# Performance work log

Hardware: AMD Instinct MI355X
Metric: run time of the kernel (lower is better)

## Reference

```python
import jax, jax.numpy as jnp
import numpy as np

B, T, DM = 2, 512, 1024
H, DH = 16, 64          # n_heads, d_head = d_model // n_heads
D, R = 32, 4            # d_manifold, metric_net rank
TEMP_MIN = 0.5


def _rope_tables(t_len, d_head):
    inv_freq = 1.0 / (10000.0 ** (jnp.arange(0, d_head, 2, dtype=jnp.float32) / d_head))
    t = jnp.arange(t_len, dtype=jnp.float32)
    freqs = t[:, None] * inv_freq[None, :]          # [T, d_head//2]
    emb = jnp.concatenate([freqs, freqs], axis=-1)  # [T, d_head]
    return jnp.cos(emb), jnp.sin(emb)


def _apply_rope(x, cos, sin):
    # x: [B, H, T, d_head]
    half = x.shape[-1] // 2
    x1, x2 = x[..., :half], x[..., half:]
    c1 = cos[None, None, :, :half]
    s1 = sin[None, None, :, :half]
    return jnp.concatenate([x1 * c1 - x2 * s1, x1 * s1 + x2 * c1], axis=-1)


def setup_inputs() -> dict:
    key = jax.random.key(0)
    ks = jax.random.split(key, 9)
    s = 0.02
    return {
        "x": jax.random.normal(ks[0], (B, T, DM), dtype=jnp.float32),
        "Wq": s * jax.random.normal(ks[1], (DM, DM), dtype=jnp.float32),
        "Wk": s * jax.random.normal(ks[2], (DM, DM), dtype=jnp.float32),
        "Wv": s * jax.random.normal(ks[3], (DM, DM), dtype=jnp.float32),
        "Wo": s * jax.random.normal(ks[4], (DM, DM), dtype=jnp.float32),
        "Wqm": s * jax.random.normal(ks[5], (DH, D), dtype=jnp.float32),
        "Wkm": s * jax.random.normal(ks[6], (DH, D), dtype=jnp.float32),
        "Wmetric": s * jax.random.normal(ks[7], (D, D * R), dtype=jnp.float32),
        "temperature": jnp.asarray(1.0, dtype=jnp.float32),
    }


def reference(x, Wq, Wk, Wv, Wo, Wqm, Wkm, Wmetric, temperature):
    b, t, c = x.shape
    # projections -> [B, H, T, d_head]
    def split_heads(y):
        return y.reshape(b, t, H, DH).transpose(0, 2, 1, 3)
    q = split_heads(x @ Wq)
    k = split_heads(x @ Wk)
    v = split_heads(x @ Wv)

    cos, sin = _rope_tables(t, DH)
    q = _apply_rope(q, cos, sin)
    k = _apply_rope(k, cos, sin)

    # manifold coordinates in (0,1): [B, H, T, D]
    qm = jax.nn.sigmoid(jnp.einsum('bhtd,dm->bhtm', q, Wqm))
    km = jax.nn.sigmoid(jnp.einsum('bhtd,dm->bhtm', k, Wkm))

    # low-rank metric factor U(q): [B, H, T, D, R]
    U = jnp.einsum('bhtm,mn->bhtn', qm, Wmetric).reshape(b, H, t, D, R)

    # Euclidean part: ||q_i - k_j||^2 = |q|^2 + |k|^2 - 2 q.k  -> [B,H,T,T]
    q2 = jnp.sum(qm * qm, axis=-1)
    k2 = jnp.sum(km * km, axis=-1)
    qk = jnp.einsum('bhid,bhjd->bhij', qm, km)
    dist_euc = q2[..., :, None] + k2[..., None, :] - 2.0 * qk

    # low-rank part: ||U_i^T (q_i - k_j)||^2, factorized as U_i^T q_i - U_i^T k_j
    Uq = jnp.einsum('bhidr,bhid->bhir', U, qm)          # [B,H,T,R]
    Uk = jnp.einsum('bhidr,bhjd->bhijr', U, km)         # [B,H,T,T,R]
    dist_lr = jnp.sum((Uq[:, :, :, None, :] - Uk) ** 2, axis=-1)

    dist_sq = jnp.maximum(dist_euc + dist_lr, 0.0)

    temp = jnp.maximum(temperature, TEMP_MIN)
    attn = -dist_sq / temp

    causal = jnp.triu(jnp.ones((t, t), dtype=bool), k=1)
    attn = jnp.where(causal[None, None], -jnp.inf, attn)
    attn = jax.nn.softmax(attn, axis=-1)

    out = jnp.einsum('bhij,bhjd->bhid', attn, v)        # [B,H,T,d_head]
    out = out.transpose(0, 2, 1, 3).reshape(b, t, c)
    return out @ Wo
```

## Files before the change

kernel.cpp:

```cpp
#include <hip/hip_runtime.h>
#include <cmath>

constexpr int B_  = 2;
constexpr int T_  = 512;
constexpr int DM_ = 1024;
constexpr int H_  = 16;
constexpr int DH_ = 64;
constexpr int D_  = 32;
constexpr int R_  = 4;
constexpr int BH_ = B_ * H_;

typedef __bf16 bf16x8 __attribute__((ext_vector_type(8)));
typedef float  f32x4  __attribute__((ext_vector_type(4)));
typedef unsigned short u16x8 __attribute__((ext_vector_type(8)));

__device__ __forceinline__ unsigned short f2bf(float f) {
    unsigned u = __float_as_uint(f);
    return (unsigned short)((u + 0x7fffu + ((u >> 16) & 1u)) >> 16);
}
__device__ __forceinline__ float bf2f(unsigned short v) {
    return __uint_as_float((unsigned)v << 16);
}
__device__ __forceinline__ void gload16(const void* g, void* l) {
    __builtin_amdgcn_global_load_lds(
        (const __attribute__((address_space(1))) void*)g,
        (__attribute__((address_space(3))) void*)l, 16, 0, 0);
}

__global__ __launch_bounds__(256) void prep_kernel(
    const float* __restrict__ x,
    const float* __restrict__ Wq, const float* __restrict__ Wk,
    const float* __restrict__ Wv, const float* __restrict__ Wo,
    unsigned short* __restrict__ xb,
    unsigned short* __restrict__ wqb, unsigned short* __restrict__ wkb,
    unsigned short* __restrict__ wvb, unsigned short* __restrict__ wob)
{
    const int t = threadIdx.x;
    const int z = blockIdx.z;
    if (z == 4) {
        int base = (blockIdx.y * 16 + blockIdx.x) * 4096 + t * 16;
#pragma unroll
        for (int c = 0; c < 4; ++c) {
            float4 v = *(const float4*)&x[base + c * 4];
            ushort4 o = { f2bf(v.x), f2bf(v.y), f2bf(v.z), f2bf(v.w) };
            *(ushort4*)&xb[base + c * 4] = o;
        }
        return;
    }
    __shared__ __align__(16) unsigned short Ls[64][72];
    const float* W = (z == 0) ? Wq : (z == 1) ? Wk : (z == 2) ? Wv : Wo;
    unsigned short* O = (z == 0) ? wqb : (z == 1) ? wkb : (z == 2) ? wvb : wob;
    const int k0 = blockIdx.x * 64;
    const int n0 = blockIdx.y * 64;
#pragma unroll
    for (int it = 0; it < 4; ++it) {
        int r = it * 16 + (t >> 4);
        int c = (t & 15) * 4;
        float4 v4 = *(const float4*)&W[(size_t)(k0 + r) * DM_ + n0 + c];
        Ls[c + 0][r] = f2bf(v4.x); Ls[c + 1][r] = f2bf(v4.y);
        Ls[c + 2][r] = f2bf(v4.z); Ls[c + 3][r] = f2bf(v4.w);
    }
    __syncthreads();
#pragma unroll
    for (int it = 0; it < 2; ++it) {
        int nl = it * 32 + (t >> 3);
        int kc = (t & 7) * 8;
        *(u16x8*)&O[(size_t)(n0 + nl) * DM_ + k0 + kc] = *(const u16x8*)&Ls[nl][kc];
    }
}

template <int EPI>
__global__ __launch_bounds__(256) void mfma_gemm_db(
    const unsigned short* __restrict__ A,
    const unsigned short* __restrict__ Bt0,
    const unsigned short* __restrict__ Bt1,
    const unsigned short* __restrict__ Bt2,
    float* __restrict__ C0, float* __restrict__ C1,
    unsigned short* __restrict__ vT)
{
    __shared__ __align__(16) unsigned short As[2][64 * 64];
    __shared__ __align__(16) unsigned short Bs[2][64 * 64];
    const int tid  = threadIdx.x;
    const int lane = tid & 63;
    const int w    = tid >> 6;
    const int wm   = (w & 1) * 32;
    const int wn   = (w >> 1) * 32;
    const int l15  = lane & 15, quad = lane >> 4;

    const int bm = blockIdx.y * 64;
    int bn, which = 0;
    const unsigned short* Bt;
    if (EPI == 0) {
        int n0 = blockIdx.x * 64;
        which = n0 >> 10;
        bn = n0 & 1023;
        Bt = (which == 0) ? Bt0 : (which == 1) ? Bt1 : Bt2;
    } else {
        bn = blockIdx.x * 64;
        Bt = Bt0;
    }

    const int srow = tid >> 3, kcs = tid & 7, kcg = kcs ^ (srow & 7);
    const unsigned short* Ap0 = A  + (size_t)(bm + srow) * DM_ + kcg * 8;
    const unsigned short* Bp0 = Bt + (size_t)(bn + srow) * DM_ + kcg * 8;
    const unsigned short* Ap1 = Ap0 + 32 * DM_;
    const unsigned short* Bp1 = Bp0 + 32 * DM_;

    gload16(Ap0, &As[0][tid * 8]);
    gload16(Ap1, &As[0][tid * 8 + 2048]);
    gload16(Bp0, &Bs[0][tid * 8]);
    gload16(Bp1, &Bs[0][tid * 8 + 2048]);

    f32x4 acc[2][2] = {};
#pragma unroll
    for (int k = 0; k < 16; ++k) {
        const int cur = k & 1, nxt = cur ^ 1;
        __builtin_amdgcn_s_barrier();
        if (k + 1 < 16) {
            const int off = (k + 1) * 64;
            gload16(Ap0 + off, &As[nxt][tid * 8]);
            gload16(Ap1 + off, &As[nxt][tid * 8 + 2048]);
            gload16(Bp0 + off, &Bs[nxt][tid * 8]);
            gload16(Bp1 + off, &Bs[nxt][tid * 8 + 2048]);
            __builtin_amdgcn_s_waitcnt(0x0F74);
        } else {
            __builtin_amdgcn_s_waitcnt(0x0F70);
        }
        __builtin_amdgcn_s_barrier();

        bf16x8 af[2][2], bfr[2][2];
#pragma unroll
        for (int ki = 0; ki < 2; ++ki)
#pragma unroll
            for (int i = 0; i < 2; ++i) {
                int ra = wm + i * 16 + l15;
                int rb = wn + i * 16 + l15;
                int kch = ki * 4 + quad;
                af[ki][i]  = *(const bf16x8*)&As[cur][ra * 64 + (kch ^ (ra & 7)) * 8];
                bfr[ki][i] = *(const bf16x8*)&Bs[cur][rb * 64 + (kch ^ (rb & 7)) * 8];
            }
#pragma unroll
        for (int mi = 0; mi < 2; ++mi)
#pragma unroll
            for (int ni = 0; ni < 2; ++ni) {
                acc[mi][ni] = __builtin_amdgcn_mfma_f32_16x16x32_bf16(
                    af[0][mi], bfr[0][ni], acc[mi][ni], 0, 0, 0);
                acc[mi][ni] = __builtin_amdgcn_mfma_f32_16x16x32_bf16(
                    af[1][mi], bfr[1][ni], acc[mi][ni], 0, 0, 0);
            }
    }

#pragma unroll
    for (int mi = 0; mi < 2; ++mi)
#pragma unroll
        for (int ni = 0; ni < 2; ++ni) {
            f32x4 a = acc[mi][ni];
            int col = wn + ni * 16 + l15;
#pragma unroll
            for (int r = 0; r < 4; ++r) {
                int row = bm + wm + mi * 16 + quad * 4 + r;
                if (EPI == 0) {
                    int h = bn >> 6, d = col;
                    int bb = row >> 9, tt = row & (T_ - 1);
                    if (which == 2) {
                        vT[(((size_t)bb * H_ + h) * DH_ + d) * T_ + tt] = f2bf(a[r]);
                    } else {
                        float* C = (which == 0) ? C0 : C1;
                        C[(((size_t)bb * H_ + h) * T_ + tt) * DH_ + d] = a[r];
                    }
                } else {
                    C0[(size_t)row * DM_ + bn + col] = a[r];
                }
            }
        }
}

__global__ __launch_bounds__(256) void feat_both(
    const float* __restrict__ q_raw, const float* __restrict__ k_raw,
    const float* __restrict__ Wqm,   const float* __restrict__ Wkm,
    const float* __restrict__ Wmetric,
    unsigned short* __restrict__ a_hi, unsigned short* __restrict__ a_lo,
    unsigned short* __restrict__ km_hi, unsigned short* __restrict__ km_lo,
    float* __restrict__ q2p, float* __restrict__ k2,
    unsigned short* __restrict__ Urb)
{
    const bool QSIDE = (blockIdx.y == 0);
    const float* raw = QSIDE ? q_raw : k_raw;
    const float* Wm  = QSIDE ? Wqm   : Wkm;

    __shared__ float qrs[4][64];
    __shared__ float qms[4][32];
    __shared__ float Us[4][128];
    __shared__ float Uqs[4][4];
    const int tid  = threadIdx.x;
    const int w    = tid >> 6;
    const int lane = tid & 63;
    const int row  = blockIdx.x * 4 + w;
    const int t    = row & (T_ - 1);
    const int bh   = row >> 9;

    float rv = raw[(size_t)row * 64 + lane];
    int   fi = lane & 31;
    float ang = (float)t * expf((float)fi * -0.28782313662425575f);
    float s, c;
    sincosf(ang, &s, &c);
    float partner = __shfl_xor(rv, 32);
    float qr = (lane < 32) ? (rv * c - partner * s) : (partner * s + rv * c);
    qrs[w][lane] = qr;
    __syncthreads();

    if (lane < 32) {
        float acc = 0.f;
#pragma unroll 8
        for (int d = 0; d < 64; ++d) acc += qrs[w][d] * Wm[d * 32 + lane];
        qms[w][lane] = 1.0f / (1.0f + __expf(-acc));
    }
    __syncthreads();

    if (QSIDE) {
        float a0 = 0.f, a1 = 0.f;
#pragma unroll 8
        for (int m = 0; m < 32; ++m) {
            float qv = qms[w][m];
            a0 += qv * Wmetric[m * 128 + lane];
            a1 += qv * Wmetric[m * 128 + 64 + lane];
        }
        Us[w][lane] = a0; Us[w][64 + lane] = a1;
        {
            int r0 = lane & 3, d0 = lane >> 2;
            int d1 = 16 + (lane >> 2);
            Urb[(((size_t)bh * R_ + r0) * T_ + t) * D_ + d0] = f2bf(a0);
            Urb[(((size_t)bh * R_ + r0) * T_ + t) * D_ + d1] = f2bf(a1);
        }
        __syncthreads();
        if (lane < 4) {
            float acc = 0.f;
#pragma unroll
            for (int d = 0; d < 32; ++d) acc += Us[w][d * 4 + lane] * qms[w][d];
            Uqs[w][lane] = acc;
        }
        __syncthreads();
        if (lane < 32) {
            float b = Uqs[w][0] * Us[w][lane * 4 + 0]
                    + Uqs[w][1] * Us[w][lane * 4 + 1]
                    + Uqs[w][2] * Us[w][lane * 4 + 2]
                    + Uqs[w][3] * Us[w][lane * 4 + 3];
            float a = qms[w][lane] + b;
            unsigned short hi = f2bf(a);
            unsigned short lo = f2bf(a - bf2f(hi));
            size_t off = (size_t)row * 32 + lane;
            a_hi[off] = hi; a_lo[off] = lo;
        }
        if (lane == 0) {
            float acc = 0.f;
#pragma unroll
            for (int m = 0; m < 32; ++m) acc += qms[w][m] * qms[w][m];
#pragma unroll
            for (int r = 0; r < 4; ++r) acc += Uqs[w][r] * Uqs[w][r];
            q2p[row] = acc;
        }
    } else {
        if (lane < 32) {
            float v = qms[w][lane];
            unsigned short hi = f2bf(v);
            unsigned short lo = f2bf(v - bf2f(hi));
            size_t off = (size_t)row * 32 + lane;
            km_hi[off] = hi; km_lo[off] = lo;
        }
        if (lane == 0) {
            float acc = 0.f;
#pragma unroll
            for (int m = 0; m < 32; ++m) acc += qms[w][m] * qms[w][m];
            k2[row] = acc;
        }
    }
}

constexpr int PROW = 40;
__global__ __launch_bounds__(256) void attn_mfma(
    const unsigned short* __restrict__ a_hi, const unsigned short* __restrict__ a_lo,
    const unsigned short* __restrict__ km_hi, const unsigned short* __restrict__ km_lo,
    const unsigned short* __restrict__ Urb,
    const float* __restrict__ q2p, const float* __restrict__ k2,
    const float* __restrict__ temp_p, const unsigned short* __restrict__ vT,
    unsigned short* __restrict__ ctxb)
{
    __shared__ __align__(16) unsigned short P_lds[4][32 * PROW];
    __shared__ __align__(16) float OP[4][32][64];
    __shared__ float ML[4][32];

    const int itile = blockIdx.x, bh = blockIdx.y;
    const int i0 = itile * 32;
    const int tid = threadIdx.x, w = tid >> 6, lane = tid & 63;
    const int l15 = lane & 15, quad = lane >> 4;

    const float inv_temp = 1.0f / fmaxf(temp_p[0], 0.5f);

    bf16x8 Ahi[2], Alo[2], Aur[4][2];
#pragma unroll
    for (int mi = 0; mi < 2; ++mi) {
        size_t ab = ((size_t)bh * T_ + i0 + mi * 16 + l15) * 32 + quad * 8;
        Ahi[mi] = *(const bf16x8*)&a_hi[ab];
        Alo[mi] = *(const bf16x8*)&a_lo[ab];
#pragma unroll
        for (int r = 0; r < 4; ++r)
            Aur[r][mi] = *(const bf16x8*)
                &Urb[(((size_t)bh * R_ + r) * T_ + i0 + mi * 16 + l15) * 32 + quad * 8];
    }
    float q2r[2][4];
#pragma unroll
    for (int mi = 0; mi < 2; ++mi)
#pragma unroll
        for (int rg = 0; rg < 4; ++rg)
            q2r[mi][rg] = q2p[(size_t)bh * T_ + i0 + mi * 16 + quad * 4 + rg];

    f32x4 Oacc[2][4] = {};
    float psum[2][4] = {};

    for (int jt = w; jt <= itile; jt += 4) {
        const int j0 = jt * 32;
        bf16x8 Bhi[2], Blo[2];
#pragma unroll
        for (int ni = 0; ni < 2; ++ni) {
            size_t kb = ((size_t)bh * T_ + j0 + ni * 16 + l15) * 32 + quad * 8;
            Bhi[ni] = *(const bf16x8*)&km_hi[kb];
            Blo[ni] = *(const bf16x8*)&km_lo[kb];
        }
        f32x4 acc[2][2] = {};
#pragma unroll
        for (int mi = 0; mi < 2; ++mi)
#pragma unroll
            for (int ni = 0; ni < 2; ++ni) {
                acc[mi][ni] = __builtin_amdgcn_mfma_f32_16x16x32_bf16(
                    Alo[mi], Bhi[ni], acc[mi][ni], 0, 0, 0);
                acc[mi][ni] = __builtin_amdgcn_mfma_f32_16x16x32_bf16(
                    Ahi[mi], Blo[ni], acc[mi][ni], 0, 0, 0);
                acc[mi][ni] = __builtin_amdgcn_mfma_f32_16x16x32_bf16(
                    Ahi[mi], Bhi[ni], acc[mi][ni], 0, 0, 0);
            }
        f32x4 sq[2][2] = {};
#pragma unroll
        for (int r = 0; r < 4; ++r) {
            f32x4 ar[2][2] = {};
#pragma unroll
            for (int mi = 0; mi < 2; ++mi)
#pragma unroll
                for (int ni = 0; ni < 2; ++ni)
                    ar[mi][ni] = __builtin_amdgcn_mfma_f32_16x16x32_bf16(
                        Aur[r][mi], Bhi[ni], ar[mi][ni], 0, 0, 0);
#pragma unroll
            for (int mi = 0; mi < 2; ++mi)
#pragma unroll
                for (int ni = 0; ni < 2; ++ni)
                    sq[mi][ni] += ar[mi][ni] * ar[mi][ni];
        }
        float k2c[2];
#pragma unroll
        for (int ni = 0; ni < 2; ++ni)
            k2c[ni] = k2[(size_t)bh * T_ + j0 + ni * 16 + l15];
        const bool diag = (jt == itile);
#pragma unroll
        for (int mi = 0; mi < 2; ++mi)
#pragma unroll
            for (int ni = 0; ni < 2; ++ni)
#pragma unroll
                for (int rg = 0; rg < 4; ++rg) {
                    float dist = q2r[mi][rg] + k2c[ni]
                               - 2.f * acc[mi][ni][rg] + sq[mi][ni][rg];
                    float sc = -fmaxf(dist, 0.f) * inv_temp;
                    if (diag && (ni * 16 + l15) > (mi * 16 + quad * 4 + rg))
                        sc = -1e30f;
                    float p = __expf(sc);
                    psum[mi][rg] += p;
                    P_lds[w][(mi * 16 + quad * 4 + rg) * PROW + ni * 16 + l15] = f2bf(p);
                }
        bf16x8 Pf[2], Vf[4];
#pragma unroll
        for (int mi = 0; mi < 2; ++mi)
            Pf[mi] = *(const bf16x8*)&P_lds[w][(mi * 16 + l15) * PROW + quad * 8];
#pragma unroll
        for (int n4 = 0; n4 < 4; ++n4)
            Vf[n4] = *(const bf16x8*)
                &vT[((size_t)bh * DH_ + n4 * 16 + l15) * T_ + j0 + quad * 8];
#pragma unroll
        for (int mi = 0; mi < 2; ++mi)
#pragma unroll
            for (int n4 = 0; n4 < 4; ++n4)
                Oacc[mi][n4] = __builtin_amdgcn_mfma_f32_16x16x32_bf16(
                    Pf[mi], Vf[n4], Oacc[mi][n4], 0, 0, 0);
    }

#pragma unroll
    for (int mi = 0; mi < 2; ++mi)
#pragma unroll
        for (int rg = 0; rg < 4; ++rg) {
            float v = psum[mi][rg];
            v += __shfl_xor(v, 1); v += __shfl_xor(v, 2);
            v += __shfl_xor(v, 4); v += __shfl_xor(v, 8);
            psum[mi][rg] = v;
        }
    if (l15 == 0)
#pragma unroll
        for (int mi = 0; mi < 2; ++mi)
#pragma unroll
            for (int rg = 0; rg < 4; ++rg)
                ML[w][mi * 16 + quad * 4 + rg] = psum[mi][rg];
#pragma unroll
    for (int mi = 0; mi < 2; ++mi)
#pragma unroll
        for (int n4 = 0; n4 < 4; ++n4)
#pragma unroll
            for (int rg = 0; rg < 4; ++rg)
                OP[w][mi * 16 + quad * 4 + rg][n4 * 16 + l15] = Oacc[mi][n4][rg];
    __syncthreads();

    const int ii = tid >> 3, ds = tid & 7;
    float l = ML[0][ii] + ML[1][ii] + ML[2][ii] + ML[3][ii];
    float O[8] = {};
#pragma unroll
    for (int wv = 0; wv < 4; ++wv) {
        float4 o0 = *(const float4*)&OP[wv][ii][ds * 8];
        float4 o1 = *(const float4*)&OP[wv][ii][ds * 8 + 4];
        O[0] += o0.x; O[1] += o0.y; O[2] += o0.z; O[3] += o0.w;
        O[4] += o1.x; O[5] += o1.y; O[6] += o1.z; O[7] += o1.w;
    }
    const float inv = 1.0f / l;
    const int b = bh >> 4, h = bh & 15;
    u16x8 o;
#pragma unroll
    for (int dd = 0; dd < 8; ++dd) o[dd] = f2bf(O[dd] * inv);
    *(u16x8*)&ctxb[((size_t)b * T_ + i0 + ii) * DM_ + h * 64 + ds * 8] = o;
}

extern "C" void kernel_launch(void* const* d_in, const int* in_sizes, int n_in,
                              void* d_out, int out_size, void* d_ws, size_t ws_size,
                              hipStream_t stream)
{
    const float* x       = (const float*)d_in[0];
    const float* Wq      = (const float*)d_in[1];
    const float* Wk      = (const float*)d_in[2];
    const float* Wv      = (const float*)d_in[3];
    const float* Wo      = (const float*)d_in[4];
    const float* Wqm     = (const float*)d_in[5];
    const float* Wkm     = (const float*)d_in[6];
    const float* Wmetric = (const float*)d_in[7];
    const float* temp    = (const float*)d_in[8];
    float* out = (float*)d_out;
    float* ws  = (float*)d_ws;

    float* q_raw = ws;
    float* k_raw = q_raw + (size_t)BH_ * T_ * DH_;
    float* q2p   = k_raw + (size_t)BH_ * T_ * DH_;
    float* k2    = q2p   + (size_t)BH_ * T_;
    unsigned short* xb   = (unsigned short*)(k2 + (size_t)BH_ * T_);
    unsigned short* wqb  = xb   + (size_t)DM_ * DM_;
    unsigned short* wkb  = wqb  + (size_t)DM_ * DM_;
    unsigned short* wvb  = wkb  + (size_t)DM_ * DM_;
    unsigned short* wob  = wvb  + (size_t)DM_ * DM_;
    unsigned short* a_hi = wob  + (size_t)DM_ * DM_;
    unsigned short* a_lo = a_hi + (size_t)BH_ * T_ * D_;
    unsigned short* kmhi = a_lo + (size_t)BH_ * T_ * D_;
    unsigned short* kmlo = kmhi + (size_t)BH_ * T_ * D_;
    unsigned short* Urb  = kmlo + (size_t)BH_ * T_ * D_;
    unsigned short* vT   = Urb  + (size_t)BH_ * R_ * T_ * D_;
    unsigned short* ctxb = (unsigned short*)q_raw;

    prep_kernel<<<dim3(16, 16, 5), 256, 0, stream>>>(
        x, Wq, Wk, Wv, Wo, xb, wqb, wkb, wvb, wob);
    mfma_gemm_db<0><<<dim3(48, 16), 256, 0, stream>>>(
        xb, wqb, wkb, wvb, q_raw, k_raw, vT);
    feat_both<<<dim3(BH_ * T_ / 4, 2), 256, 0, stream>>>(
        q_raw, k_raw, Wqm, Wkm, Wmetric,
        a_hi, a_lo, kmhi, kmlo, q2p, k2, Urb);
    attn_mfma<<<dim3(T_ / 32, BH_), 256, 0, stream>>>(
        a_hi, a_lo, kmhi, kmlo, Urb, q2p, k2, temp, vT, ctxb);
    mfma_gemm_db<1><<<dim3(16, 16), 256, 0, stream>>>(
        ctxb, wob, nullptr, nullptr, out, nullptr, nullptr);
}
```

Measured before the change: 146.9 us.

## Split-K the Q/K projection GEMM and sum partials in feature kernel

The Q and K projection GEMM tiles are split into two K-halves, each writing a separate fp32 partial buffer. The V tiles keep the full K loop. This raises the grid from 768 to 1280 blocks to fill more compute units. The feature kernel adds the two partials when it loads raw q/k. The cost is extra workspace, double the fp32 writes for q/k, and an extra read in the feature kernel. The K loop is no longer fully unrolled because the iteration count is now a runtime value.

```diff
diff --git a/kernel.cpp b/kernel.cpp
--- a/kernel.cpp
+++ b/kernel.cpp
@@ -69,13 +69,12 @@
     }
 }
 
-template <int EPI>
-__global__ __launch_bounds__(256) void mfma_gemm_db(
+__global__ __launch_bounds__(256) void qkv_gemm_ksplit(
     const unsigned short* __restrict__ A,
-    const unsigned short* __restrict__ Bt0,
-    const unsigned short* __restrict__ Bt1,
-    const unsigned short* __restrict__ Bt2,
-    float* __restrict__ C0, float* __restrict__ C1,
+    const unsigned short* __restrict__ wqb, const unsigned short* __restrict__ wkb,
+    const unsigned short* __restrict__ wvb,
+    float* __restrict__ q_rawA, float* __restrict__ q_rawB,
+    float* __restrict__ k_rawA, float* __restrict__ k_rawB,
     unsigned short* __restrict__ vT)
 {
     __shared__ __align__(16) unsigned short As[2][64 * 64];
@@ -88,17 +87,365 @@
     const int l15  = lane & 15, quad = lane >> 4;
 
     const int bm = blockIdx.y * 64;
-    int bn, which = 0;
-    const unsigned short* Bt;
-    if (EPI == 0) {
-        int n0 = blockIdx.x * 64;
+    const int u  = blockIdx.x;
+    int which, bn, k_begin, k_iters;
+    float* Cout = nullptr;
+    if (u < 64) {
+        int qk = u >> 1, half = u & 1;
+        int n0 = qk * 64;
         which = n0 >> 10;
         bn = n0 & 1023;
-        Bt = (which == 0) ? Bt0 : (which == 1) ? Bt1 : Bt2;
+        k_begin = half * 512;
+        k_iters = 8;
+        Cout = (which == 0) ? (half ? q_rawB : q_rawA)
+                            : (half ? k_rawB : k_rawA);
     } else {
-        bn = blockIdx.x * 64;
-        Bt = Bt0;
-    }
+        which = 2; bn = (u - 64) * 64; k_begin = 0; k_iters = 16;
+    }
+    const unsigned short* Bt = (which == 0) ? wqb : (which == 1) ? wkb : wvb;
+
+    const int srow = tid >> 3, kcs = tid & 7, kcg = kcs ^ (srow & 7);
+    const unsigned short* Ap0 = A  + (size_t)(bm + srow) * DM_ + kcg * 8 + k_begin;
+    const unsigned short* Bp0 = Bt + (size_t)(bn + srow) * DM_ + kcg * 8 + k_begin;
+    const unsigned short* Ap1 = Ap0 + 32 * DM_;
+    const unsigned short* Bp1 = Bp0 + 32 * DM_;
+
+    gload16(Ap0, &As[0][tid * 8]);
+    gload16(Ap1, &As[0][tid * 8 + 2048]);
+    gload16(Bp0, &Bs[0][tid * 8]);
+    gload16(Bp1, &Bs[0][tid * 8 + 2048]);
+
+    f32x4 acc[2][2] = {};
+    for (int k = 0; k < k_iters; ++k) {
+        const int cur = k & 1, nxt = cur ^ 1;
+        __builtin_amdgcn_s_barrier();
+        if (k + 1 < k_iters) {
+            const int off = (k + 1) * 64;
+            gload16(Ap0 + off, &As[nxt][tid * 8]);
+            gload16(Ap1 + off, &As[nxt][tid * 8 + 2048]);
+            gload16(Bp0 + off, &Bs[nxt][tid * 8]);
+            gload16(Bp1 + off, &Bs[nxt][tid * 8 + 2048]);
+            __builtin_amdgcn_s_waitcnt(0x0F74);
+        } else {
+            __builtin_amdgcn_s_waitcnt(0x0F70);
+        }
+        __builtin_amdgcn_s_barrier();
+
+        bf16x8 af[2][2], bfr[2][2];
+#pragma unroll
+        for (int ki = 0; ki < 2; ++ki)
+#pragma unroll
+            for (int i = 0; i < 2; ++i) {
+                int ra = wm + i * 16 + l15;
+                int rb = wn + i * 16 + l15;
+                int kch = ki * 4 + quad;
+                af[ki][i]  = *(const bf16x8*)&As[cur][ra * 64 + (kch ^ (ra & 7)) * 8];
+                bfr[ki][i] = *(const bf16x8*)&Bs[cur][rb * 64 + (kch ^ (rb & 7)) * 8];
+            }
+#pragma unroll
+        for (int mi = 0; mi < 2; ++mi)
+#pragma unroll
+            for (int ni = 0; ni < 2; ++ni) {
+                acc[mi][ni] = __builtin_amdgcn_mfma_f32_16x16x32_bf16(
+                    af[0][mi], bfr[0][ni], acc[mi][ni], 0, 0, 0);
+                acc[mi][ni] = __builtin_amdgcn_mfma_f32_16x16x32_bf16(
+                    af[1][mi], bfr[1][ni], acc[mi][ni], 0, 0, 0);
+            }
+    }
+
+    const int h = bn >> 6;
+#pragma unroll
+    for (int mi = 0; mi < 2; ++mi)
+#pragma unroll
+        for (int ni = 0; ni < 2; ++ni) {
+            f32x4 a = acc[mi][ni];
+            int d = wn + ni * 16 + l15;
+#pragma unroll
+            for (int r = 0; r < 4; ++r) {
+                int row = bm + wm + mi * 16 + quad * 4 + r;
+                int bb = row >> 9, tt = row & (T_ - 1);
+                if (which == 2) {
+                    vT[(((size_t)bb * H_ + h) * DH_ + d) * T_ + tt] = f2bf(a[r]);
+                } else {
+                    Cout[(((size_t)bb * H_ + h) * T_ + tt) * DH_ + d] = a[r];
+                }
+            }
+        }
+}
+
+__global__ __launch_bounds__(256) void feat_both(
+    const float* __restrict__ q_rawA, const float* __restrict__ q_rawB,
+    const float* __restrict__ k_rawA, const float* __restrict__ k_rawB,
+    const float* __restrict__ Wqm,   const float* __restrict__ Wkm,
+    const float* __restrict__ Wmetric,
+    unsigned short* __restrict__ a_hi, unsigned short* __restrict__ a_lo,
+    unsigned short* __restrict__ km_hi, unsigned short* __restrict__ km_lo,
+    float* __restrict__ q2p, float* __restrict__ k2,
+    unsigned short* __restrict__ Urb)
+{
+    const bool QSIDE = (blockIdx.y == 0);
+    const float* rawA = QSIDE ? q_rawA : k_rawA;
+    const float* rawB = QSIDE ? q_rawB : k_rawB;
+    const float* Wm   = QSIDE ? Wqm   : Wkm;
+
+    __shared__ float qrs[4][64];
+    __shared__ float qms[4][32];
+    __shared__ float Us[4][128];
+    __shared__ float Uqs[4][4];
+    const int tid  = threadIdx.x;
+    const int w    = tid >> 6;
+    const int lane = tid & 63;
+    const int row  = blockIdx.x * 4 + w;
+    const int t    = row & (T_ - 1);
+    const int bh   = row >> 9;
+
+    float rv = rawA[(size_t)row * 64 + lane] + rawB[(size_t)row * 64 + lane];
+    int   fi = lane & 31;
+    float ang = (float)t * expf((float)fi * -0.28782313662425575f);
+    float s, c;
+    sincosf(ang, &s, &c);
+    float partner = __shfl_xor(rv, 32);
+    float qr = (lane < 32) ? (rv * c - partner * s) : (partner * s + rv * c);
+    qrs[w][lane] = qr;
+    __syncthreads();
+
+    if (lane < 32) {
+        float acc = 0.f;
+#pragma unroll 8
+        for (int d = 0; d < 64; ++d) acc += qrs[w][d] * Wm[d * 32 + lane];
+        qms[w][lane] = 1.0f / (1.0f + __expf(-acc));
+    }
+    __syncthreads();
+
+    if (QSIDE) {
+        float a0 = 0.f, a1 = 0.f;
+#pragma unroll 8
+        for (int m = 0; m < 32; ++m) {
+            float qv = qms[w][m];
+            a0 += qv * Wmetric[m * 128 + lane];
+            a1 += qv * Wmetric[m * 128 + 64 + lane];
+        }
+        Us[w][lane] = a0; Us[w][64 + lane] = a1;
+        {
+            int r0 = lane & 3, d0 = lane >> 2;
+            int d1 = 16 + (lane >> 2);
+            Urb[(((size_t)bh * R_ + r0) * T_ + t) * D_ + d0] = f2bf(a0);
+            Urb[(((size_t)bh * R_ + r0) * T_ + t) * D_ + d1] = f2bf(a1);
+        }
+        __syncthreads();
+        if (lane < 4) {
+            float acc = 0.f;
+#pragma unroll
+            for (int d = 0; d < 32; ++d) acc += Us[w][d * 4 + lane] * qms[w][d];
+            Uqs[w][lane] = acc;
+        }
+        __syncthreads();
+        if (lane < 32) {
+            float b = Uqs[w][0] * Us[w][lane * 4 + 0]
+                    + Uqs[w][1] * Us[w][lane * 4 + 1]
+                    + Uqs[w][2] * Us[w][lane * 4 + 2]
+                    + Uqs[w][3] * Us[w][lane * 4 + 3];
+            float a = qms[w][lane] + b;
+            unsigned short hi = f2bf(a);
+            unsigned short lo = f2bf(a - bf2f(hi));
+            size_t off = (size_t)row * 32 + lane;
+            a_hi[off] = hi; a_lo[off] = lo;
+        }
+        if (lane == 0) {
+            float acc = 0.f;
+#pragma unroll
+            for (int m = 0; m < 32; ++m) acc += qms[w][m] * qms[w][m];
+#pragma unroll
+            for (int r = 0; r < 4; ++r) acc += Uqs[w][r] * Uqs[w][r];
+            q2p[row] = acc;
+        }
+    } else {
+        if (lane < 32) {
+            float v = qms[w][lane];
+            unsigned short hi = f2bf(v);
+            unsigned short lo = f2bf(v - bf2f(hi));
+            size_t off = (size_t)row * 32 + lane;
+            km_hi[off] = hi; km_lo[off] = lo;
+        }
+        if (lane == 0) {
+            float acc = 0.f;
+#pragma unroll
+            for (int m = 0; m < 32; ++m) acc += qms[w][m] * qms[w][m];
+            k2[row] = acc;
+        }
+    }
+}
+
+constexpr int PROW = 40;
+__global__ __launch_bounds__(256) void attn_mfma(
+    const unsigned short* __restrict__ a_hi, const unsigned short* __restrict__ a_lo,
+    const unsigned short* __restrict__ km_hi, const unsigned short* __restrict__ km_lo,
+    const unsigned short* __restrict__ Urb,
+    const float* __restrict__ q2p, const float* __restrict__ k2,
+    const float* __restrict__ temp_p, const unsigned short* __restrict__ vT,
+    unsigned short* __restrict__ ctxb)
+{
+    __shared__ __align__(16) unsigned short P_lds[4][32 * PROW];
+    __shared__ __align__(16) float OP[4][32][64];
+    __shared__ float ML[4][32];
+
+    const int itile = blockIdx.x, bh = blockIdx.y;
+    const int i0 = itile * 32;
+    const int tid = threadIdx.x, w = tid >> 6, lane = tid & 63;
+    const int l15 = lane & 15, quad = lane >> 4;
+
+    const float inv_temp = 1.0f / fmaxf(temp_p[0], 0.5f);
+
+    bf16x8 Ahi[2], Alo[2], Aur[4][2];
+#pragma unroll
+    for (int mi = 0; mi < 2; ++mi) {
+        size_t ab = ((size_t)bh * T_ + i0 + mi * 16 + l15) * 32 + quad * 8;
+        Ahi[mi] = *(const bf16x8*)&a_hi[ab];
+        Alo[mi] = *(const bf16x8*)&a_lo[ab];
+#pragma unroll
+        for (int r = 0; r < 4; ++r)
+            Aur[r][mi] = *(const bf16x8*)
+                &Urb[(((size_t)bh * R_ + r) * T_ + i0 + mi * 16 + l15) * 32 + quad * 8];
+    }
+    float q2r[2][4];
+#pragma unroll
+    for (int mi = 0; mi < 2; ++mi)
+#pragma unroll
+        for (int rg = 0; rg < 4; ++rg)
+            q2r[mi][rg] = q2p[(size_t)bh * T_ + i0 + mi * 16 + quad * 4 + rg];
+
+    f32x4 Oacc[2][4] = {};
+    float psum[2][4] = {};
+
+    for (int jt = w; jt <= itile; jt += 4) {
+        const int j0 = jt * 32;
+        bf16x8 Bhi[2], Blo[2];
+#pragma unroll
+        for (int ni = 0; ni < 2; ++ni) {
+            size_t kb = ((size_t)bh * T_ + j0 + ni * 16 + l15) * 32 + quad * 8;
+            Bhi[ni] = *(const bf16x8*)&km_hi[kb];
+            Blo[ni] = *(const bf16x8*)&km_lo[kb];
+        }
+        f32x4 acc[2][2] = {};
+#pragma unroll
+        for (int mi = 0; mi < 2; ++mi)
+#pragma unroll
+            for (int ni = 0; ni < 2; ++ni) {
+                acc[mi][ni] = __builtin_amdgcn_mfma_f32_16x16x32_bf16(
+                    Alo[mi], Bhi[ni], acc[mi][ni], 0, 0, 0);
+                acc[mi][ni] = __builtin_amdgcn_mfma_f32_16x16x32_bf16(
+                    Ahi[mi], Blo[ni], acc[mi][ni], 0, 0, 0);
+                acc[mi][ni] = __builtin_amdgcn_mfma_f32_16x16x32_bf16(
+                    Ahi[mi], Bhi[ni], acc[mi][ni], 0, 0, 0);
+            }
+        f32x4 sq[2][2] = {};
+#pragma unroll
+        for (int r = 0; r < 4; ++r) {
+            f32x4 ar[2][2] = {};
+#pragma unroll
+            for (int mi = 0; mi < 2; ++mi)
+#pragma unroll
+                for (int ni = 0; ni < 2; ++ni)
+                    ar[mi][ni] = __builtin_amdgcn_mfma_f32_16x16x32_bf16(
+                        Aur[r][mi], Bhi[ni], ar[mi][ni], 0, 0, 0);
+#pragma unroll
+            for (int mi = 0; mi < 2; ++mi)
+#pragma unroll
+                for (int ni = 0; ni < 2; ++ni)
+                    sq[mi][ni] += ar[mi][ni] * ar[mi][ni];
+        }
+        float k2c[2];
+#pragma unroll
+        for (int ni = 0; ni < 2; ++ni)
+            k2c[ni] = k2[(size_t)bh * T_ + j0 + ni * 16 + l15];
+        const bool diag = (jt == itile);
+#pragma unroll
+        for (int mi = 0; mi < 2; ++mi)
+#pragma unroll
+            for (int ni = 0; ni < 2; ++ni)
+#pragma unroll
+                for (int rg = 0; rg < 4; ++rg) {
+                    float dist = q2r[mi][rg] + k2c[ni]
+                               - 2.f * acc[mi][ni][rg] + sq[mi][ni][rg];
+                    float sc = -fmaxf(dist, 0.f) * inv_temp;
+                    if (diag && (ni * 16 + l15) > (mi * 16 + quad * 4 + rg))
+                        sc = -1e30f;
+                    float p = __expf(sc);
+                    psum[mi][rg] += p;
+                    P_lds[w][(mi * 16 + quad * 4 + rg) * PROW + ni * 16 + l15] = f2bf(p);
+                }
+        bf16x8 Pf[2], Vf[4];
+#pragma unroll
+        for (int mi = 0; mi < 2; ++mi)
+            Pf[mi] = *(const bf16x8*)&P_lds[w][(mi * 16 + l15) * PROW + quad * 8];
+#pragma unroll
+        for (int n4 = 0; n4 < 4; ++n4)
+            Vf[n4] = *(const bf16x8*)
+                &vT[((size_t)bh * DH_ + n4 * 16 + l15) * T_ + j0 + quad * 8];
+#pragma unroll
+        for (int mi = 0; mi < 2; ++mi)
+#pragma unroll
+            for (int n4 = 0; n4 < 4; ++n4)
+                Oacc[mi][n4] = __builtin_amdgcn_mfma_f32_16x16x32_bf16(
+                    Pf[mi], Vf[n4], Oacc[mi][n4], 0, 0, 0);
+    }
+
+#pragma unroll
+    for (int mi = 0; mi < 2; ++mi)
+#pragma unroll
+        for (int rg = 0; rg < 4; ++rg) {
+            float v = psum[mi][rg];
+            v += __shfl_xor(v, 1); v += __shfl_xor(v, 2);
+            v += __shfl_xor(v, 4); v += __shfl_xor(v, 8);
+            psum[mi][rg] = v;
+        }
+    if (l15 == 0)
+#pragma unroll
+        for (int mi = 0; mi < 2; ++mi)
+#pragma unroll
+            for (int rg = 0; rg < 4; ++rg)
+                ML[w][mi * 16 + quad * 4 + rg] = psum[mi][rg];
+#pragma unroll
+    for (int mi = 0; mi < 2; ++mi)
+#pragma unroll
+        for (int n4 = 0; n4 < 4; ++n4)
+#pragma unroll
+            for (int rg = 0; rg < 4; ++rg)
+                OP[w][mi * 16 + quad * 4 + rg][n4 * 16 + l15] = Oacc[mi][n4][rg];
+    __syncthreads();
+
+    const int ii = tid >> 3, ds = tid & 7;
+    float l = ML[0][ii] + ML[1][ii] + ML[2][ii] + ML[3][ii];
+    float O[8] = {};
+#pragma unroll
+    for (int wv = 0; wv < 4; ++wv) {
+        float4 o0 = *(const float4*)&OP[wv][ii][ds * 8];
+        float4 o1 = *(const float4*)&OP[wv][ii][ds * 8 + 4];
+        O[0] += o0.x; O[1] += o0.y; O[2] += o0.z; O[3] += o0.w;
+        O[4] += o1.x; O[5] += o1.y; O[6] += o1.z; O[7] += o1.w;
+    }
+    const float inv = 1.0f / l;
+    const int b = bh >> 4, h = bh & 15;
+    u16x8 o;
+#pragma unroll
+    for (int dd = 0; dd < 8; ++dd) o[dd] = f2bf(O[dd] * inv);
+    *(u16x8*)&ctxb[((size_t)b * T_ + i0 + ii) * DM_ + h * 64 + ds * 8] = o;
+}
+
+__global__ __launch_bounds__(256) void out_gemm_db(
+    const unsigned short* __restrict__ A, const unsigned short* __restrict__ Bt,
+    float* __restrict__ C)
+{
+    __shared__ __align__(16) unsigned short As[2][64 * 64];
+    __shared__ __align__(16) unsigned short Bs[2][64 * 64];
+    const int tid  = threadIdx.x;
+    const int lane = tid & 63;
+    const int w    = tid >> 6;
+    const int wm   = (w & 1) * 32;
+    const int wn   = (w >> 1) * 32;
+    const int l15  = lane & 15, quad = lane >> 4;
+    const int bm = blockIdx.y * 64;
+    const int bn = blockIdx.x * 64;
 
     const int srow = tid >> 3, kcs = tid & 7, kcg = kcs ^ (srow & 7);
     const unsigned short* Ap0 = A  + (size_t)(bm + srow) * DM_ + kcg * 8;
@@ -112,7 +459,6 @@
     gload16(Bp1, &Bs[0][tid * 8 + 2048]);
 
     f32x4 acc[2][2] = {};
-#pragma unroll
     for (int k = 0; k < 16; ++k) {
         const int cur = k & 1, nxt = cur ^ 1;
         __builtin_amdgcn_s_barrier();
@@ -149,287 +495,18 @@
                     af[1][mi], bfr[1][ni], acc[mi][ni], 0, 0, 0);
             }
     }
-
 #pragma unroll
     for (int mi = 0; mi < 2; ++mi)
 #pragma unroll
         for (int ni = 0; ni < 2; ++ni) {
             f32x4 a = acc[mi][ni];
-            int col = wn + ni * 16 + l15;
+            int col = bn + wn + ni * 16 + l15;
 #pragma unroll
             for (int r = 0; r < 4; ++r) {
                 int row = bm + wm + mi * 16 + quad * 4 + r;
-                if (EPI == 0) {
-                    int h = bn >> 6, d = col;
-                    int bb = row >> 9, tt = row & (T_ - 1);
-                    if (which == 2) {
-                        vT[(((size_t)bb * H_ + h) * DH_ + d) * T_ + tt] = f2bf(a[r]);
-                    } else {
-                        float* C = (which == 0) ? C0 : C1;
-                        C[(((size_t)bb * H_ + h) * T_ + tt) * DH_ + d] = a[r];
-                    }
-                } else {
-                    C0[(size_t)row * DM_ + bn + col] = a[r];
-                }
-            }
-        }
-}
-
-__global__ __launch_bounds__(256) void feat_both(
-    const float* __restrict__ q_raw, const float* __restrict__ k_raw,
-    const float* __restrict__ Wqm,   const float* __restrict__ Wkm,
-    const float* __restrict__ Wmetric,
-    unsigned short* __restrict__ a_hi, unsigned short* __restrict__ a_lo,
-    unsigned short* __restrict__ km_hi, unsigned short* __restrict__ km_lo,
-    float* __restrict__ q2p, float* __restrict__ k2,
-    unsigned short* __restrict__ Urb)
-{
-    const bool QSIDE = (blockIdx.y == 0);
-    const float* raw = QSIDE ? q_raw : k_raw;
-    const float* Wm  = QSIDE ? Wqm   : Wkm;
-
-    __shared__ float qrs[4][64];
-    __shared__ float qms[4][32];
-    __shared__ float Us[4][128];
-    __shared__ float Uqs[4][4];
-    const int tid  = threadIdx.x;
-    const int w    = tid >> 6;
-    const int lane = tid & 63;
-    const int row  = blockIdx.x * 4 + w;
-    const int t    = row & (T_ - 1);
-    const int bh   = row >> 9;
-
-    float rv = raw[(size_t)row * 64 + lane];
-    int   fi = lane & 31;
-    float ang = (float)t * expf((float)fi * -0.28782313662425575f);
-    float s, c;
-    sincosf(ang, &s, &c);
-    float partner = __shfl_xor(rv, 32);
-    float qr = (lane < 32) ? (rv * c - partner * s) : (partner * s + rv * c);
-    qrs[w][lane] = qr;
-    __syncthreads();
-
-    if (lane < 32) {
-        float acc = 0.f;
-#pragma unroll 8
-        for (int d = 0; d < 64; ++d) acc += qrs[w][d] * Wm[d * 32 + lane];
-        qms[w][lane] = 1.0f / (1.0f + __expf(-acc));
-    }
-    __syncthreads();
-
-    if (QSIDE) {
-        float a0 = 0.f, a1 = 0.f;
-#pragma unroll 8
-        for (int m = 0; m < 32; ++m) {
-            float qv = qms[w][m];
-            a0 += qv * Wmetric[m * 128 + lane];
-            a1 += qv * Wmetric[m * 128 + 64 + lane];
-        }
-        Us[w][lane] = a0; Us[w][64 + lane] = a1;
-        {
-            int r0 = lane & 3, d0 = lane >> 2;
-            int d1 = 16 + (lane >> 2);
-            Urb[(((size_t)bh * R_ + r0) * T_ + t) * D_ + d0] = f2bf(a0);
-            Urb[(((size_t)bh * R_ + r0) * T_ + t) * D_ + d1] = f2bf(a1);
-        }
-        __syncthreads();
-        if (lane < 4) {
-            float acc = 0.f;
-#pragma unroll
-            for (int d = 0; d < 32; ++d) acc += Us[w][d * 4 + lane] * qms[w][d];
-            Uqs[w][lane] = acc;
-        }
-        __syncthreads();
-        if (lane < 32) {
-            float b = Uqs[w][0] * Us[w][lane * 4 + 0]
-                    + Uqs[w][1] * Us[w][lane * 4 + 1]
-                    + Uqs[w][2] * Us[w][lane * 4 + 2]
-                    + Uqs[w][3] * Us[w][lane * 4 + 3];
-            float a = qms[w][lane] + b;
-            unsigned short hi = f2bf(a);
-            unsigned short lo = f2bf(a - bf2f(hi));
-            size_t off = (size_t)row * 32 + lane;
-            a_hi[off] = hi; a_lo[off] = lo;
-        }
-        if (lane == 0) {
-            float acc = 0.f;
-#pragma unroll
-            for (int m = 0; m < 32; ++m) acc += qms[w][m] * qms[w][m];
-#pragma unroll
-            for (int r = 0; r < 4; ++r) acc += Uqs[w][r] * Uqs[w][r];
-            q2p[row] = acc;
-        }
-    } else {
-        if (lane < 32) {
-            float v = qms[w][lane];
-            unsigned short hi = f2bf(v);
-            unsigned short lo = f2bf(v - bf2f(hi));
-            size_t off = (size_t)row * 32 + lane;
-            km_hi[off] = hi; km_lo[off] = lo;
-        }
-        if (lane == 0) {
-            float acc = 0.f;
-#pragma unroll
-            for (int m = 0; m < 32; ++m) acc += qms[w][m] * qms[w][m];
-            k2[row] = acc;
-        }
-    }
-}
-
-constexpr int PROW = 40;
-__global__ __launch_bounds__(256) void attn_mfma(
-    const unsigned short* __restrict__ a_hi, const unsigned short* __restrict__ a_lo,
-    const unsigned short* __restrict__ km_hi, const unsigned short* __restrict__ km_lo,
-    const unsigned short* __restrict__ Urb,
-    const float* __restrict__ q2p, const float* __restrict__ k2,
-    const float* __restrict__ temp_p, const unsigned short* __restrict__ vT,
-    unsigned short* __restrict__ ctxb)
-{
-    __shared__ __align__(16) unsigned short P_lds[4][32 * PROW];
-    __shared__ __align__(16) float OP[4][32][64];
-    __shared__ float ML[4][32];
-
-    const int itile = blockIdx.x, bh = blockIdx.y;
-    const int i0 = itile * 32;
-    const int tid = threadIdx.x, w = tid >> 6, lane = tid & 63;
-    const int l15 = lane & 15, quad = lane >> 4;
-
-    const float inv_temp = 1.0f / fmaxf(temp_p[0], 0.5f);
-
-    bf16x8 Ahi[2], Alo[2], Aur[4][2];
-#pragma unroll
-    for (int mi = 0; mi < 2; ++mi) {
-        size_t ab = ((size_t)bh * T_ + i0 + mi * 16 + l15) * 32 + quad * 8;
-        Ahi[mi] = *(const bf16x8*)&a_hi[ab];
-        Alo[mi] = *(const bf16x8*)&a_lo[ab];
-#pragma unroll
-        for (int r = 0; r < 4; ++r)
-            Aur[r][mi] = *(const bf16x8*)
-                &Urb[(((size_t)bh * R_ + r) * T_ + i0 + mi * 16 + l15) * 32 + quad * 8];
-    }
-    float q2r[2][4];
-#pragma unroll
-    for (int mi = 0; mi < 2; ++mi)
-#pragma unroll
-        for (int rg = 0; rg < 4; ++rg)
-            q2r[mi][rg] = q2p[(size_t)bh * T_ + i0 + mi * 16 + quad * 4 + rg];
-
-    f32x4 Oacc[2][4] = {};
-    float psum[2][4] = {};
-
-    for (int jt = w; jt <= itile; jt += 4) {
-        const int j0 = jt * 32;
-        bf16x8 Bhi[2], Blo[2];
-#pragma unroll
-        for (int ni = 0; ni < 2; ++ni) {
-            size_t kb = ((size_t)bh * T_ + j0 + ni * 16 + l15) * 32 + quad * 8;
-            Bhi[ni] = *(const bf16x8*)&km_hi[kb];
-            Blo[ni] = *(const bf16x8*)&km_lo[kb];
-        }
-        f32x4 acc[2][2] = {};
-#pragma unroll
-        for (int mi = 0; mi < 2; ++mi)
-#pragma unroll
-            for (int ni = 0; ni < 2; ++ni) {
-                acc[mi][ni] = __builtin_amdgcn_mfma_f32_16x16x32_bf16(
-                    Alo[mi], Bhi[ni], acc[mi][ni], 0, 0, 0);
-                acc[mi][ni] = __builtin_amdgcn_mfma_f32_16x16x32_bf16(
-                    Ahi[mi], Blo[ni], acc[mi][ni], 0, 0, 0);
-                acc[mi][ni] = __builtin_amdgcn_mfma_f32_16x16x32_bf16(
-                    Ahi[mi], Bhi[ni], acc[mi][ni], 0, 0, 0);
-            }
-        f32x4 sq[2][2] = {};
-#pragma unroll
-        for (int r = 0; r < 4; ++r) {
-            f32x4 ar[2][2] = {};
-#pragma unroll
-            for (int mi = 0; mi < 2; ++mi)
-#pragma unroll
-                for (int ni = 0; ni < 2; ++ni)
-                    ar[mi][ni] = __builtin_amdgcn_mfma_f32_16x16x32_bf16(
-                        Aur[r][mi], Bhi[ni], ar[mi][ni], 0, 0, 0);
-#pragma unroll
-            for (int mi = 0; mi < 2; ++mi)
-#pragma unroll
-                for (int ni = 0; ni < 2; ++ni)
-                    sq[mi][ni] += ar[mi][ni] * ar[mi][ni];
-        }
-        float k2c[2];
-#pragma unroll
-        for (int ni = 0; ni < 2; ++ni)
-            k2c[ni] = k2[(size_t)bh * T_ + j0 + ni * 16 + l15];
-        const bool diag = (jt == itile);
-#pragma unroll
-        for (int mi = 0; mi < 2; ++mi)
-#pragma unroll
-            for (int ni = 0; ni < 2; ++ni)
-#pragma unroll
-                for (int rg = 0; rg < 4; ++rg) {
-                    float dist = q2r[mi][rg] + k2c[ni]
-                               - 2.f * acc[mi][ni][rg] + sq[mi][ni][rg];
-                    float sc = -fmaxf(dist, 0.f) * inv_temp;
-                    if (diag && (ni * 16 + l15) > (mi * 16 + quad * 4 + rg))
-                        sc = -1e30f;
-                    float p = __expf(sc);
-                    psum[mi][rg] += p;
-                    P_lds[w][(mi * 16 + quad * 4 + rg) * PROW + ni * 16 + l15] = f2bf(p);
-                }
-        bf16x8 Pf[2], Vf[4];
-#pragma unroll
-        for (int mi = 0; mi < 2; ++mi)
-            Pf[mi] = *(const bf16x8*)&P_lds[w][(mi * 16 + l15) * PROW + quad * 8];
-#pragma unroll
-        for (int n4 = 0; n4 < 4; ++n4)
-            Vf[n4] = *(const bf16x8*)
-                &vT[((size_t)bh * DH_ + n4 * 16 + l15) * T_ + j0 + quad * 8];
-#pragma unroll
-        for (int mi = 0; mi < 2; ++mi)
-#pragma unroll
-            for (int n4 = 0; n4 < 4; ++n4)
-                Oacc[mi][n4] = __builtin_amdgcn_mfma_f32_16x16x32_bf16(
-                    Pf[mi], Vf[n4], Oacc[mi][n4], 0, 0, 0);
-    }
-
-#pragma unroll
-    for (int mi = 0; mi < 2; ++mi)
-#pragma unroll
-        for (int rg = 0; rg < 4; ++rg) {
-            float v = psum[mi][rg];
-            v += __shfl_xor(v, 1); v += __shfl_xor(v, 2);
-            v += __shfl_xor(v, 4); v += __shfl_xor(v, 8);
-            psum[mi][rg] = v;
-        }
-    if (l15 == 0)
-#pragma unroll
-        for (int mi = 0; mi < 2; ++mi)
-#pragma unroll
-            for (int rg = 0; rg < 4; ++rg)
-                ML[w][mi * 16 + quad * 4 + rg] = psum[mi][rg];
-#pragma unroll
-    for (int mi = 0; mi < 2; ++mi)
-#pragma unroll
-        for (int n4 = 0; n4 < 4; ++n4)
-#pragma unroll
-            for (int rg = 0; rg < 4; ++rg)
-                OP[w][mi * 16 + quad * 4 + rg][n4 * 16 + l15] = Oacc[mi][n4][rg];
-    __syncthreads();
-
-    const int ii = tid >> 3, ds = tid & 7;
-    float l = ML[0][ii] + ML[1][ii] + ML[2][ii] + ML[3][ii];
-    float O[8] = {};
-#pragma unroll
-    for (int wv = 0; wv < 4; ++wv) {
-        float4 o0 = *(const float4*)&OP[wv][ii][ds * 8];
-        float4 o1 = *(const float4*)&OP[wv][ii][ds * 8 + 4];
-        O[0] += o0.x; O[1] += o0.y; O[2] += o0.z; O[3] += o0.w;
-        O[4] += o1.x; O[5] += o1.y; O[6] += o1.z; O[7] += o1.w;
-    }
-    const float inv = 1.0f / l;
-    const int b = bh >> 4, h = bh & 15;
-    u16x8 o;
-#pragma unroll
-    for (int dd = 0; dd < 8; ++dd) o[dd] = f2bf(O[dd] * inv);
-    *(u16x8*)&ctxb[((size_t)b * T_ + i0 + ii) * DM_ + h * 64 + ds * 8] = o;
+                C[(size_t)row * DM_ + col] = a[r];
+            }
+        }
 }
 
 extern "C" void kernel_launch(void* const* d_in, const int* in_sizes, int n_in,
@@ -448,10 +525,12 @@
     float* out = (float*)d_out;
     float* ws  = (float*)d_ws;
 
-    float* q_raw = ws;
-    float* k_raw = q_raw + (size_t)BH_ * T_ * DH_;
-    float* q2p   = k_raw + (size_t)BH_ * T_ * DH_;
-    float* k2    = q2p   + (size_t)BH_ * T_;
+    float* q_rawA = ws;
+    float* q_rawB = q_rawA + (size_t)BH_ * T_ * DH_;
+    float* k_rawA = q_rawB + (size_t)BH_ * T_ * DH_;
+    float* k_rawB = k_rawA + (size_t)BH_ * T_ * DH_;
+    float* q2p    = k_rawB + (size_t)BH_ * T_ * DH_;
+    float* k2     = q2p    + (size_t)BH_ * T_;
     unsigned short* xb   = (unsigned short*)(k2 + (size_t)BH_ * T_);
     unsigned short* wqb  = xb   + (size_t)DM_ * DM_;
     unsigned short* wkb  = wqb  + (size_t)DM_ * DM_;
@@ -463,17 +542,16 @@
     unsigned short* kmlo = kmhi + (size_t)BH_ * T_ * D_;
     unsigned short* Urb  = kmlo + (size_t)BH_ * T_ * D_;
     unsigned short* vT   = Urb  + (size_t)BH_ * R_ * T_ * D_;
-    unsigned short* ctxb = (unsigned short*)q_raw;
+    unsigned short* ctxb = (unsigned short*)q_rawA;
 
     prep_kernel<<<dim3(16, 16, 5), 256, 0, stream>>>(
         x, Wq, Wk, Wv, Wo, xb, wqb, wkb, wvb, wob);
-    mfma_gemm_db<0><<<dim3(48, 16), 256, 0, stream>>>(
-        xb, wqb, wkb, wvb, q_raw, k_raw, vT);
+    qkv_gemm_ksplit<<<dim3(80, 16), 256, 0, stream>>>(
+        xb, wqb, wkb, wvb, q_rawA, q_rawB, k_rawA, k_rawB, vT);
     feat_both<<<dim3(BH_ * T_ / 4, 2), 256, 0, stream>>>(
-        q_raw, k_raw, Wqm, Wkm, Wmetric,
+        q_rawA, q_rawB, k_rawA, k_rawB, Wqm, Wkm, Wmetric,
         a_hi, a_lo, kmhi, kmlo, q2p, k2, Urb);
     attn_mfma<<<dim3(T_ / 32, BH_), 256, 0, stream>>>(
         a_hi, a_lo, kmhi, kmlo, Urb, q2p, k2, temp, vT, ctxb);
-    mfma_gemm_db<1><<<dim3(16, 16), 256, 0, stream>>>(
-        ctxb, wob, nullptr, nullptr, out, nullptr, nullptr);
-}
+    out_gemm_db<<<dim3(16, 16), 256, 0, stream>>>(ctxb, wob, out);
+}
```

After: 155.9 us. 6.1% more time.
